# Performance work log

Measured on AMD Instinct MI355X. Metric: run time of the kernel, lower is better.

## Reference

```python
import jax, jax.numpy as jnp
import numpy as np

# Conv config (matches init_kwargs): 3x3 conv, 256->256, stride 1, pad 1
KH, KW = 3, 3
STRIDE = (1, 1)
PAD = ((1, 1), (1, 1))


def setup_inputs() -> dict:
    key = jax.random.key(0)
    k1, k2, k3 = jax.random.split(key, 3)
    x = jax.random.normal(k1, (32, 256, 56, 56), dtype=jnp.float32)
    # linear.weight = conv.weight.view(C_out, C_in*kH*kW) -> [256, 2304]
    weight = jax.random.normal(k2, (256, 256 * KH * KW), dtype=jnp.float32) * 0.02
    bias = jax.random.normal(k3, (256,), dtype=jnp.float32)
    return {"x": x, "weight": weight, "bias": bias}


def reference(x, weight, bias):
    # im2col (same layout/order as F.unfold: feature dim = C * kH * kW, c-major)
    # patches: [N, C*kH*kW, H_out, W_out]
    patches = jax.lax.conv_general_dilated_patches(
        x, filter_shape=(KH, KW), window_strides=STRIDE, padding=PAD
    )
    # dense GEMM over the unfolded feature dim (the nn.Linear)
    y = jnp.einsum("nkhw,ok->nohw", patches, weight)
    y = y + bias[None, :, None, None]
    return y
```

## Files before the change

### kernel.cpp

```cpp
#include <hip/hip_runtime.h>
#include <hip/hip_bf16.h>

typedef short bf16x8 __attribute__((ext_vector_type(8)));
typedef float f32x4  __attribute__((ext_vector_type(4)));
typedef unsigned int uint4v __attribute__((ext_vector_type(4)));

#define HWHW   3136
#define ROWSH  40
#define ROWBYTES 80

__device__ __forceinline__ unsigned short f2bf(float f) {
    unsigned int u = __float_as_uint(f);
    u += 0x7fffu + ((u >> 16) & 1u);
    return (unsigned short)(u >> 16);
}

__global__ void wprep(const float* __restrict__ w, unsigned short* __restrict__ wt) {
    int idx = blockIdx.x * blockDim.x + threadIdx.x;
    int e    = idx & 7;
    int lane = (idx >> 3) & 63;
    int om   = (idx >> 9) & 15;
    int c8   = (idx >> 13) & 7;
    int t    = idx >> 16;
    int o = om * 16 + (lane & 15);
    int c = c8 * 32 + (lane >> 4) * 8 + e;
    wt[idx] = f2bf(w[o * 2304 + c * 9 + t]);
}

__global__ void xprep(const float* __restrict__ x, unsigned short* __restrict__ xt) {
    const int hp = blockIdx.x;
    const int c8 = blockIdx.y;
    const int n  = blockIdx.z;
    const int t  = threadIdx.x;
    const int wp  = t >> 2;
    const int ccq = t & 3;
    const int h = hp - 1, w = wp - 1;
    const bool ok = (h >= 0) && (h < 56) && (w >= 0) && (w < 56);
    const int sp = ok ? (h * 56 + w) : 0;
    const float* xr = x + ((size_t)n * 256 + c8 * 32 + ccq * 8) * HWHW + sp;
    uint4v d;
#pragma unroll
    for (int p = 0; p < 4; ++p) {
        float f0 = ok ? xr[(size_t)(2 * p) * HWHW] : 0.0f;
        float f1 = ok ? xr[(size_t)(2 * p + 1) * HWHW] : 0.0f;
        d[p] = (unsigned)f2bf(f0) | ((unsigned)f2bf(f1) << 16);
    }
    *(uint4v*)(xt + ((((size_t)n * 8 + c8) * 58 + hp) * 2048) + wp * 32 + ccq * 8) = d;
}

__global__ __launch_bounds__(256, 2)
void conv_main(const unsigned short* __restrict__ xt, const unsigned short* __restrict__ wt,
               const float* __restrict__ bias, float* __restrict__ out) {
    __shared__ __align__(16) short xs[2][6 * 64 * ROWSH];

    const int bx = blockIdx.x;
    const int hb = bx >> 1;
    const int bm = bx & 1;
    const int n  = blockIdx.y;
    const int h0 = hb * 4;

    const int tid  = threadIdx.x;
    const int lane = tid & 63;
    const int wv   = tid >> 6;
    const int wm   = wv & 1;
    const int ng   = wv >> 1;
    const int g    = lane >> 4;
    const int lcol = lane & 15;

    int bboff[7][3];
#pragma unroll
    for (int f = 0; f < 7; ++f) {
        int j = ng * 112 + f * 16 + lcol;
        int r = j / 56, wc = j % 56;
#pragma unroll
        for (int kw = 0; kw < 3; ++kw) {
            int ww  = wc + kw;
            int bit = (ww >> 3) & 1;
            bboff[f][kw] = (r * 64 + ww) * ROWBYTES + 16 * (g ^ bit);
        }
    }

    const int sg  = tid & 3;
    const int swp = (tid >> 2) & 63;
    const int swb = swp * ROWBYTES + 16 * (sg ^ ((swp >> 3) & 1));

    const unsigned short* wl = wt + (size_t)lane * 8;
    const int obase = bm * 8 + wm * 4;

    f32x4 acc[4][7];
#pragma unroll
    for (int m = 0; m < 4; ++m)
#pragma unroll
        for (int f = 0; f < 7; ++f) acc[m][f] = (f32x4){0.f, 0.f, 0.f, 0.f};

    bf16x8 sv[6];
    auto s_load = [&](int c8) {
        const unsigned short* p = xt + (((size_t)n * 8 + c8) * 58 + h0) * 2048 + swp * 32 + sg * 8;
#pragma unroll
        for (int r = 0; r < 6; ++r) sv[r] = *(const bf16x8*)(p + (size_t)r * 2048);
    };
    auto s_write = [&](int buf) {
        char* d = (char*)&xs[buf][0] + swb;
#pragma unroll
        for (int r = 0; r < 6; ++r)
            *(bf16x8*)(d + r * 64 * ROWBYTES) = sv[r];
    };

    s_load(0);
    s_write(0);
    __syncthreads();

    for (int c8 = 0; c8 < 8; ++c8) {
        const bool more = c8 < 7;
        if (more) s_load(c8 + 1);
        const char* xb = (const char*)&xs[c8 & 1][0];

        bf16x8 a0[4], a1[4];
#pragma unroll
        for (int m = 0; m < 4; ++m)
            a0[m] = *(const bf16x8*)(wl + (size_t)((c8 * 16) + obase + m) * 512);

#pragma unroll
        for (int t = 0; t < 9; ++t) {
            bf16x8* ac = (t & 1) ? a1 : a0;
            bf16x8* an = (t & 1) ? a0 : a1;
            if (t < 8) {
#pragma unroll
                for (int m = 0; m < 4; ++m)
                    an[m] = *(const bf16x8*)(wl + (size_t)((((t + 1) * 8 + c8) * 16) + obase + m) * 512);
            }
            const int kh = t / 3, kw = t % 3;
            const int dt = kh * 64 * ROWBYTES;
#pragma unroll
            for (int f = 0; f < 7; ++f) {
                bf16x8 b = *(const bf16x8*)(xb + bboff[f][kw] + dt);
#pragma unroll
                for (int m = 0; m < 4; ++m)
                    acc[m][f] = __builtin_amdgcn_mfma_f32_16x16x32_bf16(ac[m], b, acc[m][f], 0, 0, 0);
            }
        }

        if (more) s_write((c8 + 1) & 1);
        __syncthreads();
    }

#pragma unroll
    for (int m = 0; m < 4; ++m) {
#pragma unroll
        for (int q = 0; q < 4; ++q) {
            int o = bm * 128 + wm * 64 + m * 16 + 4 * g + q;
            float bs = bias[o];
            float* yo = out + ((size_t)n * 256 + o) * HWHW + hb * 224;
#pragma unroll
            for (int f = 0; f < 7; ++f) {
                int j = ng * 112 + f * 16 + lcol;
                yo[j] = acc[m][f][q] + bs;
            }
        }
    }
}

__global__ __launch_bounds__(512, 2)
void conv_fallback(const float* __restrict__ x, const unsigned short* __restrict__ wt,
                   const float* __restrict__ bias, float* __restrict__ out) {
    __shared__ short xs[2][348 * 40];
    const int hb = blockIdx.x, n = blockIdx.y, h0 = hb * 4;
    const int tid = threadIdx.x, lane = tid & 63, wv = tid >> 6;
    const int wm = wv & 3, ng = wv >> 2, g = lane >> 4, lcol = lane & 15;
    int bbase[7];
#pragma unroll
    for (int f = 0; f < 7; ++f) {
        int j = ng * 112 + f * 16 + lcol;
        bbase[f] = ((j / 56) * 58 + (j % 56)) * 40 + 8 * g;
    }
    const int cpair = tid >> 5, col0 = tid & 31;
    const float* xn = x + (size_t)n * 256 * HWHW;
    float sv0[6][2], sv1[6][2];
    f32x4 acc[4][7];
#pragma unroll
    for (int m = 0; m < 4; ++m)
#pragma unroll
        for (int f = 0; f < 7; ++f) acc[m][f] = (f32x4){0.f, 0.f, 0.f, 0.f};
    const unsigned short* wl = wt + (size_t)lane * 8;
    auto stage_load = [&](int c8) {
        const float* xc0 = xn + (size_t)(c8 * 32 + 2 * cpair) * HWHW;
        const float* xc1 = xc0 + HWHW;
#pragma unroll
        for (int r = 0; r < 6; ++r) {
            int hh = h0 - 1 + r;
            bool rok = (hh >= 0) & (hh < 56);
#pragma unroll
            for (int ci = 0; ci < 2; ++ci) {
                int col = col0 + 32 * ci, ww = col - 1;
                bool ok = rok & (col < 58) & (ww >= 0) & (ww < 56);
                int off = hh * 56 + ww;
                sv0[r][ci] = ok ? xc0[off] : 0.0f;
                sv1[r][ci] = ok ? xc1[off] : 0.0f;
            }
        }
    };
    auto stage_write = [&](int buf) {
#pragma unroll
        for (int r = 0; r < 6; ++r)
#pragma unroll
            for (int ci = 0; ci < 2; ++ci) {
                int col = col0 + 32 * ci;
                if (col < 58) {
                    unsigned int p = (unsigned int)f2bf(sv0[r][ci]) |
                                     ((unsigned int)f2bf(sv1[r][ci]) << 16);
                    *(unsigned int*)&xs[buf][(r * 58 + col) * 40 + 2 * cpair] = p;
                }
            }
    };
    stage_load(0); stage_write(0);
    __syncthreads();
    for (int c8 = 0; c8 < 8; ++c8) {
        if (c8 < 7) stage_load(c8 + 1);
        const short* xb = &xs[c8 & 1][0];
        bf16x8 a0[4], a1[4];
#pragma unroll
        for (int m = 0; m < 4; ++m)
            a0[m] = *(const bf16x8*)(wl + (size_t)((c8 * 16) + 4 * wm + m) * 512);
#pragma unroll
        for (int t = 0; t < 9; ++t) {
            bf16x8* ac = (t & 1) ? a1 : a0;
            bf16x8* an = (t & 1) ? a0 : a1;
            if (t < 8) {
#pragma unroll
                for (int m = 0; m < 4; ++m)
                    an[m] = *(const bf16x8*)(wl + (size_t)((((t + 1) * 8 + c8) * 16) + 4 * wm + m) * 512);
            }
            const int dt = ((t / 3) * 58 + (t % 3)) * 40;
#pragma unroll
            for (int f = 0; f < 7; ++f) {
                bf16x8 b = *(const bf16x8*)&xb[bbase[f] + dt];
#pragma unroll
                for (int m = 0; m < 4; ++m)
                    acc[m][f] = __builtin_amdgcn_mfma_f32_16x16x32_bf16(ac[m], b, acc[m][f], 0, 0, 0);
            }
        }
        if (c8 < 7) stage_write((c8 + 1) & 1);
        __syncthreads();
    }
#pragma unroll
    for (int m = 0; m < 4; ++m) {
#pragma unroll
        for (int q = 0; q < 4; ++q) {
            int o = 64 * wm + 16 * m + 4 * g + q;
            float bs = bias[o];
            float* yo = out + ((size_t)n * 256 + o) * HWHW + h0 * 56;
#pragma unroll
            for (int f = 0; f < 7; ++f) {
                int j = ng * 112 + f * 16 + lcol;
                yo[j] = acc[m][f][q] + bs;
            }
        }
    }
}

extern "C" void kernel_launch(void* const* d_in, const int* in_sizes, int n_in,
                              void* d_out, int out_size, void* d_ws, size_t ws_size,
                              hipStream_t stream) {
    const float* x    = (const float*)d_in[0];
    const float* w    = (const float*)d_in[1];
    const float* bias = (const float*)d_in[2];
    float* out        = (float*)d_out;
    unsigned short* wt = (unsigned short*)d_ws;
    unsigned short* xtp = (unsigned short*)((char*)d_ws + 1179648);

    wprep<<<2304, 256, 0, stream>>>(w, wt);
    if (ws_size >= (size_t)1179648 + 60817408) {
        xprep<<<dim3(58, 8, 32), 256, 0, stream>>>(x, xtp);
        conv_main<<<dim3(28, 32), 256, 0, stream>>>(xtp, wt, bias, out);
    } else {
        conv_fallback<<<dim3(14, 32), 512, 0, stream>>>(x, wt, bias, out);
    }
}
```

Measured before the change: 146.1 us.

## Swizzle block order for XCD locality and pipeline weight loads across channel chunks

The 2D grid becomes a 1D grid of 896 blocks. Block IDs are remapped so that consecutive blocks on the same XCD (bid & 7) handle contiguous (n, h-band) tiles, which should improve L2 reuse of the transformed input and weights. The channel-chunk loop is unrolled by two with parity-tracked double buffers, so the first weight fragment of the next chunk is prefetched during the last tap of the current chunk. The LDS write for the next chunk moves up to after tap 3 so it overlaps with the MFMA work. Together these aim to hide global-load latency at chunk boundaries, at the cost of higher register pressure and more code size.

```diff
diff --git a/kernel.cpp b/kernel.cpp
--- a/kernel.cpp
+++ b/kernel.cpp
@@ -53,10 +53,12 @@
                const float* __restrict__ bias, float* __restrict__ out) {
     __shared__ __align__(16) short xs[2][6 * 64 * ROWSH];
 
-    const int bx = blockIdx.x;
-    const int hb = bx >> 1;
-    const int bm = bx & 1;
-    const int n  = blockIdx.y;
+    const int bid  = blockIdx.x;
+    const int bid2 = (bid & 7) * 112 + (bid >> 3);
+    const int n  = bid2 / 28;
+    const int r2 = bid2 % 28;
+    const int hb = r2 >> 1;
+    const int bm = r2 & 1;
     const int h0 = hb * 4;
 
     const int tid  = threadIdx.x;
@@ -105,44 +107,49 @@
         for (int r = 0; r < 6; ++r)
             *(bf16x8*)(d + r * 64 * ROWBYTES) = sv[r];
     };
-
+    auto a_load = [&](bf16x8* dst, int c8, int t) {
+#pragma unroll
+        for (int m = 0; m < 4; ++m)
+            dst[m] = *(const bf16x8*)(wl + (size_t)((t * 8 + c8) * 16 + obase + m) * 512);
+    };
+
+    bf16x8 aA[4], aB[4];
+
+#define CHUNK_BODY(C8, PAR, MORE) do {                                          \
+    const bool more_ = (MORE);                                                  \
+    if (more_) s_load((C8) + 1);          \
+    const char* xb = (const char*)&xs[(C8) & 1][0];                             \
+    _Pragma("unroll")                                                           \
+    for (int t = 0; t < 9; ++t) {                                               \
+        bf16x8* ac = (((t + (PAR)) & 1) ? aB : aA);                             \
+        bf16x8* an = (((t + (PAR)) & 1) ? aA : aB);                             \
+        if (t < 8)      a_load(an, (C8), t + 1);                                \
+        else if (more_) a_load(an, (C8) + 1, 0);          \
+        const int kh = t / 3, kw = t % 3;                                       \
+        const int dt = kh * 64 * ROWBYTES;                                      \
+        _Pragma("unroll")                                                       \
+        for (int f = 0; f < 7; ++f) {                                           \
+            bf16x8 b = *(const bf16x8*)(xb + bboff[f][kw] + dt);                \
+            _Pragma("unroll")                                                   \
+            for (int m = 0; m < 4; ++m)                                         \
+                acc[m][f] = __builtin_amdgcn_mfma_f32_16x16x32_bf16(ac[m], b, acc[m][f], 0, 0, 0); \
+        }                                                                       \
+        if (t == 3 && more_) s_write(((C8) + 1) & 1);      \
+    }                                                                           \
+    __syncthreads();                                                            \
+} while (0)
+
+    a_load(aA, 0, 0);
     s_load(0);
     s_write(0);
     __syncthreads();
 
-    for (int c8 = 0; c8 < 8; ++c8) {
-        const bool more = c8 < 7;
-        if (more) s_load(c8 + 1);
-        const char* xb = (const char*)&xs[c8 & 1][0];
-
-        bf16x8 a0[4], a1[4];
-#pragma unroll
-        for (int m = 0; m < 4; ++m)
-            a0[m] = *(const bf16x8*)(wl + (size_t)((c8 * 16) + obase + m) * 512);
-
-#pragma unroll
-        for (int t = 0; t < 9; ++t) {
-            bf16x8* ac = (t & 1) ? a1 : a0;
-            bf16x8* an = (t & 1) ? a0 : a1;
-            if (t < 8) {
-#pragma unroll
-                for (int m = 0; m < 4; ++m)
-                    an[m] = *(const bf16x8*)(wl + (size_t)((((t + 1) * 8 + c8) * 16) + obase + m) * 512);
-            }
-            const int kh = t / 3, kw = t % 3;
-            const int dt = kh * 64 * ROWBYTES;
-#pragma unroll
-            for (int f = 0; f < 7; ++f) {
-                bf16x8 b = *(const bf16x8*)(xb + bboff[f][kw] + dt);
-#pragma unroll
-                for (int m = 0; m < 4; ++m)
-                    acc[m][f] = __builtin_amdgcn_mfma_f32_16x16x32_bf16(ac[m], b, acc[m][f], 0, 0, 0);
-            }
-        }
-
-        if (more) s_write((c8 + 1) & 1);
-        __syncthreads();
-    }
+    for (int c4 = 0; c4 < 4; ++c4) {
+        const int c8e = 2 * c4;
+        CHUNK_BODY(c8e, 0, true);
+        CHUNK_BODY(c8e + 1, 1, c8e + 1 < 7);
+    }
+#undef CHUNK_BODY
 
 #pragma unroll
     for (int m = 0; m < 4; ++m) {
@@ -271,7 +278,7 @@
     wprep<<<2304, 256, 0, stream>>>(w, wt);
     if (ws_size >= (size_t)1179648 + 60817408) {
         xprep<<<dim3(58, 8, 32), 256, 0, stream>>>(x, xtp);
-        conv_main<<<dim3(28, 32), 256, 0, stream>>>(xtp, wt, bias, out);
+        conv_main<<<896, 256, 0, stream>>>(xtp, wt, bias, out);
     } else {
         conv_fallback<<<dim3(14, 32), 512, 0, stream>>>(x, wt, bias, out);
     }
```

New measurement: 190.4 us. 30.3% more time.
